# Kernel tuning notes

Measured on AMD Instinct MI355X. Metric: run time of the kernel, lower is better.

Reference implementation:

```python
import jax, jax.numpy as jnp
import numpy as np

N_TOTAL = 100000  # total nodes in feature table
N = 16384         # batch of center nodes
K = 32            # fixed neighbor count per relation
S = 16            # num_sample = ceil(K * threshold=0.5)
D = 190           # feat_dim (hard-coded in source weight)
E = 64            # embed_dim


def setup_inputs() -> dict:
    key = jax.random.key(0)
    ks = jax.random.split(key, 7)
    features = jax.random.normal(ks[0], (N_TOTAL, D), dtype=jnp.float32)
    nodes = jax.random.randint(ks[1], (N,), 0, N_TOTAL)
    neigh1 = jax.random.randint(ks[2], (N, K), 0, N_TOTAL)
    neigh2 = jax.random.randint(ks[3], (N, K), 0, N_TOTAL)
    neigh3 = jax.random.randint(ks[4], (N, K), 0, N_TOTAL)
    lim_w = float(np.sqrt(6.0 / (D + E)))  # xavier_uniform
    weight = jax.random.uniform(ks[5], (D, E), minval=-lim_w, maxval=lim_w, dtype=jnp.float32)
    lim_a = float(np.sqrt(6.0 / (2 * E + 1)))
    a = jax.random.uniform(ks[6], (2 * E, 1), minval=-lim_a, maxval=lim_a, dtype=jnp.float32)
    return {"features": features, "nodes": nodes, "neigh1": neigh1,
            "neigh2": neigh2, "neigh3": neigh3, "weight": weight, "a": a}


def _intra(features, nodes, neigh):
    """Cosine-similarity top-S neighbor filter + masked mean + relu (IntraAgg)."""
    center = features[nodes]                      # [N, D]
    nf = features[neigh]                          # [N, K, D] gather
    sim = jnp.einsum('nd,nkd->nk', center, nf)
    sim = sim / (jnp.linalg.norm(center, axis=1, keepdims=True)
                 * jnp.linalg.norm(nf, axis=2))   # cosine similarity [N, K]
    _, top_idx = jax.lax.top_k(sim, S)            # [N, S] most-similar neighbors
    sel = jnp.take_along_axis(nf, top_idx[:, :, None], axis=1)  # [N, S, D]
    return jax.nn.relu(sel.mean(axis=1))          # uniform average -> relu, [N, D]


def reference(features, nodes, neigh1, neigh2, neigh3, weight, a):
    r_feats = [_intra(features, nodes, nb) for nb in (neigh1, neigh2, neigh3)]
    self_feats = features[nodes]                  # [N, D]
    center_h = self_feats @ weight                # [N, E]
    neigh_h = jnp.stack([r @ weight for r in r_feats])  # [3, N, E]
    # cat(center_h, neigh_h) @ a == center_h @ a[:E] + neigh_h @ a[E:]
    a1, a2 = a[:E], a[E:]
    e = jax.nn.leaky_relu(center_h @ a1 + neigh_h @ a2, 0.2)  # [3, N, 1]
    att = jax.nn.softmax(e[..., 0].T, axis=1)     # [N, 3] (eval mode: no dropout)
    aggregated = jnp.einsum('nr,rne->ne', att, neigh_h)       # [N, E]
    return jax.nn.relu(center_h + aggregated)
```

## Files before the change

### kernel.cpp

```cpp
#include <hip/hip_runtime.h>

#define NTOTAL 100000
#define NNODES 16384
#define K 32
#define S 16
#define D 190
#define E 64
#define NREL 3

__device__ float g_invn[NTOTAL];
__device__ float g_wa[384];

__global__ __launch_bounds__(256) void norms_kernel(const float* __restrict__ features) {
    const int row  = blockIdx.x * 4 + (threadIdx.x >> 6);
    const int lane = threadIdx.x & 63;
    if (row >= NTOTAL) return;
    const float2* rp = (const float2*)(features + (size_t)row * D);
    float2 a = rp[lane];
    float ss = fmaf(a.x, a.x, a.y * a.y);
    if (lane < 31) {
        float2 b = rp[64 + lane];
        ss = fmaf(b.x, b.x, fmaf(b.y, b.y, ss));
    }
    #pragma unroll
    for (int off = 32; off; off >>= 1) ss += __shfl_xor(ss, off, 64);
    if (lane == 0) g_invn[row] = 1.0f / sqrtf(ss);
}

__global__ __launch_bounds__(192) void prep_wa(const float* __restrict__ weight,
                                               const float* __restrict__ avec) {
    const int d = threadIdx.x;
    float s1 = 0.f, s2 = 0.f;
    if (d < D) {
        const float* wr = weight + d * E;
        #pragma unroll 8
        for (int e = 0; e < E; ++e) {
            const float w = wr[e];
            s1 = fmaf(w, avec[e],     s1);
            s2 = fmaf(w, avec[E + e], s2);
        }
    }
    g_wa[d]       = s1;
    g_wa[192 + d] = s2;
}

__global__ __launch_bounds__(256) void interagg_wave(
    const float* __restrict__ features,
    const int*   __restrict__ nodes,
    const int*   __restrict__ neigh1,
    const int*   __restrict__ neigh2,
    const int*   __restrict__ neigh3,
    const float* __restrict__ weight,
    float*       __restrict__ out)
{
    __shared__ int   s_idx[4][96];
    __shared__ float s_sim[4][32];
    __shared__ __align__(16) float s_v[4][192];

    const int t    = threadIdx.x;
    const int lane = t & 63;
    const int wave = t >> 6;
    const int n    = blockIdx.x * 4 + wave;

    int*   idxw = s_idx[wave];
    float* simw = s_sim[wave];
    float* vw   = s_v[wave];

    {
        const int v1 = (lane < 32) ? neigh1[n * K + lane] : neigh2[n * K + (lane - 32)];
        idxw[lane] = v1;
        if (lane < 32) idxw[64 + lane] = neigh3[n * K + lane];
    }

    const int  crow = nodes[n];
    const int  hl   = (lane < 31) ? lane : 30;
    const bool hiok = (lane < 31);
    const float2* crp = (const float2*)(features + (size_t)crow * D);
    float2 c0 = crp[lane];
    float2 c1 = crp[64 + hl];
    if (!hiok) { c1.x = 0.f; c1.y = 0.f; }

    float rlx[NREL], rly[NREL], rhx[NREL], rhy[NREL];

    #pragma unroll
    for (int rel = 0; rel < NREL; ++rel) {
        const int* idz = idxw + rel * 32;

        #pragma unroll
        for (int b = 0; b < 4; ++b) {
            float2 va[8], vb[8];
            float  dt[8];
            #pragma unroll
            for (int i = 0; i < 8; ++i) {
                const int rid = idz[b * 8 + i];
                const float2* rp = (const float2*)(features + (size_t)rid * D);
                va[i] = rp[lane];
                vb[i] = rp[64 + hl];
            }
            #pragma unroll
            for (int i = 0; i < 8; ++i)
                dt[i] = fmaf(c0.x, va[i].x, fmaf(c0.y, va[i].y,
                        fmaf(c1.x, vb[i].x, c1.y * vb[i].y)));
            #pragma unroll
            for (int off = 32; off; off >>= 1) {
                #pragma unroll
                for (int i = 0; i < 8; ++i)
                    dt[i] += __shfl_xor(dt[i], off, 64);
            }
            if (lane == 0) {
                #pragma unroll
                for (int i = 0; i < 8; ++i)
                    simw[b * 8 + i] = dt[i];
            }
        }

        if (lane < 32) simw[lane] *= g_invn[idz[lane]];

        const float sk = simw[lane & 31];
        int rank = (lane < 32) ? 0 : 64;
        #pragma unroll
        for (int j = 0; j < K; ++j) {
            const float sj = __shfl(sk, j, 64);
            rank += (sj > sk) || (sj == sk && j < lane);
        }
        unsigned int m = (unsigned int)__ballot(rank < S);

        float2 acc_lo = make_float2(0.f, 0.f);
        float2 acc_hi = make_float2(0.f, 0.f);
        #pragma unroll
        for (int half = 0; half < 2; ++half) {
            float2 ua[8], ub[8];
            #pragma unroll
            for (int i = 0; i < 8; ++i) {
                const int k = __ffs(m) - 1; m &= m - 1;
                const int rid = idz[k];
                const float2* rp = (const float2*)(features + (size_t)rid * D);
                ua[i] = rp[lane];
                ub[i] = rp[64 + hl];
            }
            #pragma unroll
            for (int i = 0; i < 8; ++i) {
                acc_lo.x += ua[i].x; acc_lo.y += ua[i].y;
                acc_hi.x += ub[i].x; acc_hi.y += ub[i].y;
            }
        }
        rlx[rel] = fmaxf(acc_lo.x * (1.f / S), 0.f);
        rly[rel] = fmaxf(acc_lo.y * (1.f / S), 0.f);
        rhx[rel] = fmaxf(acc_hi.x * (1.f / S), 0.f);
        rhy[rel] = fmaxf(acc_hi.y * (1.f / S), 0.f);
    }

    float2 w1l = ((const float2*)g_wa)[lane];
    float2 w1h = ((const float2*)g_wa)[64 + hl];
    float2 w2l = ((const float2*)(g_wa + 192))[lane];
    float2 w2h = ((const float2*)(g_wa + 192))[64 + hl];
    if (!hiok) { w1h.x = w1h.y = 0.f; w2h.x = w2h.y = 0.f; }

    float dv[4];
    dv[0] = fmaf(c0.x, w1l.x, fmaf(c0.y, w1l.y, fmaf(c1.x, w1h.x, c1.y * w1h.y)));
    #pragma unroll
    for (int r = 0; r < NREL; ++r)
        dv[1 + r] = fmaf(rlx[r], w2l.x, fmaf(rly[r], w2l.y,
                    fmaf(rhx[r], w2h.x, rhy[r] * w2h.y)));
    #pragma unroll
    for (int off = 32; off; off >>= 1) {
        #pragma unroll
        for (int i = 0; i < 4; ++i)
            dv[i] += __shfl_xor(dv[i], off, 64);
    }

    float e1 = dv[0] + dv[1], e2 = dv[0] + dv[2], e3 = dv[0] + dv[3];
    e1 = (e1 >= 0.f) ? e1 : 0.2f * e1;
    e2 = (e2 >= 0.f) ? e2 : 0.2f * e2;
    e3 = (e3 >= 0.f) ? e3 : 0.2f * e3;
    const float mx  = fmaxf(e1, fmaxf(e2, e3));
    const float x1 = expf(e1 - mx), x2 = expf(e2 - mx), x3 = expf(e3 - mx);
    const float inv = 1.f / (x1 + x2 + x3);
    const float a1w = x1 * inv, a2w = x2 * inv, a3w = x3 * inv;

    float2 v_lo, v_hi;
    v_lo.x = fmaf(a1w, rlx[0], fmaf(a2w, rlx[1], fmaf(a3w, rlx[2], c0.x)));
    v_lo.y = fmaf(a1w, rly[0], fmaf(a2w, rly[1], fmaf(a3w, rly[2], c0.y)));
    v_hi.x = fmaf(a1w, rhx[0], fmaf(a2w, rhx[1], fmaf(a3w, rhx[2], c1.x)));
    v_hi.y = fmaf(a1w, rhy[0], fmaf(a2w, rhy[1], fmaf(a3w, rhy[2], c1.y)));

    ((float2*)vw)[lane] = v_lo;
    if (hiok) ((float2*)vw)[64 + lane] = v_hi;

    float acc = 0.f;
    const float* wcol = weight + lane;
    #pragma unroll 4
    for (int d4 = 0; d4 < 47; ++d4) {
        const float4 vv = *((const float4*)vw + d4);
        const int d = d4 * 4;
        acc = fmaf(vv.x, wcol[(d    ) * E], acc);
        acc = fmaf(vv.y, wcol[(d + 1) * E], acc);
        acc = fmaf(vv.z, wcol[(d + 2) * E], acc);
        acc = fmaf(vv.w, wcol[(d + 3) * E], acc);
    }
    {
        const float2 vv2 = *((const float2*)vw + 94);
        acc = fmaf(vv2.x, wcol[188 * E], acc);
        acc = fmaf(vv2.y, wcol[189 * E], acc);
    }
    out[(size_t)n * E + lane] = fmaxf(acc, 0.f);
}

extern "C" void kernel_launch(void* const* d_in, const int* in_sizes, int n_in,
                              void* d_out, int out_size, void* d_ws, size_t ws_size,
                              hipStream_t stream) {
    const float* features = (const float*)d_in[0];
    const int*   nodes    = (const int*)  d_in[1];
    const int*   neigh1   = (const int*)  d_in[2];
    const int*   neigh2   = (const int*)  d_in[3];
    const int*   neigh3   = (const int*)  d_in[4];
    const float* weight   = (const float*)d_in[5];
    const float* avec     = (const float*)d_in[6];
    float*       out      = (float*)d_out;

    norms_kernel<<<NTOTAL / 4, 256, 0, stream>>>(features);
    prep_wa<<<1, 192, 0, stream>>>(weight, avec);
    interagg_wave<<<NNODES / 4, 256, 0, stream>>>(
        features, nodes, neigh1, neigh2, neigh3, weight, out);
}
```

Before: 319.9 us.

## Pad feature rows to 192 floats in workspace and embed inverse norm

Adds a pre-pass that copies the feature table into a workspace with rows padded to 192 floats, storing each row's inverse norm in the padding slot. The main kernel gathers from the padded, aligned rows and takes the norm from a lane it already loads, so the separate norm lookup goes away. This costs an extra full-table write pass and depends on having enough workspace, with the old path kept as a fallback.

After: 468.3 us. 1.46x slower.

```diff
diff --git a/kernel.cpp b/kernel.cpp
--- a/kernel.cpp
+++ b/kernel.cpp
@@ -7,9 +7,29 @@
 #define D 190
 #define E 64
 #define NREL 3
+#define PROW 192
 
 __device__ float g_invn[NTOTAL];
 __device__ float g_wa[384];
+
+__global__ __launch_bounds__(256) void pad_kernel(const float* __restrict__ features,
+                                                  float* __restrict__ pf) {
+    const int row  = blockIdx.x * 4 + (threadIdx.x >> 6);
+    const int lane = threadIdx.x & 63;
+    if (row >= NTOTAL) return;
+    const float2* rp = (const float2*)(features + (size_t)row * D);
+    float2 lo = rp[lane];
+    float2 hi = make_float2(0.f, 0.f);
+    if (lane < 31) hi = rp[64 + lane];
+    float ss = fmaf(lo.x, lo.x, fmaf(lo.y, lo.y, fmaf(hi.x, hi.x, hi.y * hi.y)));
+    #pragma unroll
+    for (int off = 32; off; off >>= 1) ss += __shfl_xor(ss, off, 64);
+    const float invn = 1.0f / sqrtf(ss);
+    float2* wp = (float2*)(pf + (size_t)row * PROW);
+    wp[lane] = lo;
+    if (lane < 31) wp[64 + lane] = hi;
+    if (lane == 31) wp[95] = make_float2(invn, 0.f);
+}
 
 __global__ __launch_bounds__(256) void norms_kernel(const float* __restrict__ features) {
     const int row  = blockIdx.x * 4 + (threadIdx.x >> 6);
@@ -42,6 +62,167 @@
     }
     g_wa[d]       = s1;
     g_wa[192 + d] = s2;
+}
+
+__global__ __launch_bounds__(256) void interagg_pad(
+    const float* __restrict__ pf,
+    const int*   __restrict__ nodes,
+    const int*   __restrict__ neigh1,
+    const int*   __restrict__ neigh2,
+    const int*   __restrict__ neigh3,
+    const float* __restrict__ weight,
+    float*       __restrict__ out)
+{
+    __shared__ int   s_idx[4][96];
+    __shared__ float s_sim[4][32];
+    __shared__ __align__(16) float s_v[4][192];
+
+    const int t    = threadIdx.x;
+    const int lane = t & 63;
+    const int wave = t >> 6;
+    const int n    = blockIdx.x * 4 + wave;
+
+    int*   idxw = s_idx[wave];
+    float* simw = s_sim[wave];
+    float* vw   = s_v[wave];
+
+    {
+        const int v1 = (lane < 32) ? neigh1[n * K + lane] : neigh2[n * K + (lane - 32)];
+        idxw[lane] = v1;
+        if (lane < 32) idxw[64 + lane] = neigh3[n * K + lane];
+    }
+
+    const int  crow = nodes[n];
+    const bool hiok = (lane < 32);
+    const float2* crp = (const float2*)(pf + (size_t)crow * PROW);
+    float2 c0 = crp[lane];
+    float2 c1 = hiok ? crp[64 + lane] : make_float2(0.f, 0.f);
+    if (lane == 31) { c1.x = 0.f; c1.y = 0.f; }
+
+    float rlx[NREL], rly[NREL], rhx[NREL], rhy[NREL];
+
+    #pragma unroll
+    for (int rel = 0; rel < NREL; ++rel) {
+        const int* idz = idxw + rel * 32;
+
+        #pragma unroll
+        for (int b = 0; b < 4; ++b) {
+            float2 va[8], vb[8];
+            float  dt[8];
+            #pragma unroll
+            for (int i = 0; i < 8; ++i) {
+                const int rid = idz[b * 8 + i];
+                const float2* rp = (const float2*)(pf + (size_t)rid * PROW);
+                va[i] = rp[lane];
+                vb[i] = hiok ? rp[64 + lane] : make_float2(0.f, 0.f);
+            }
+            #pragma unroll
+            for (int i = 0; i < 8; ++i) {
+                dt[i] = fmaf(c0.x, va[i].x, fmaf(c0.y, va[i].y,
+                        fmaf(c1.x, vb[i].x, c1.y * vb[i].y)));
+            }
+            #pragma unroll
+            for (int off = 32; off; off >>= 1) {
+                #pragma unroll
+                for (int i = 0; i < 8; ++i)
+                    dt[i] += __shfl_xor(dt[i], off, 64);
+            }
+            if (lane == 31) {
+                #pragma unroll
+                for (int i = 0; i < 8; ++i)
+                    simw[b * 8 + i] = dt[i] * vb[i].x;
+            }
+        }
+
+        const float sk = simw[lane & 31];
+        int rank = (lane < 32) ? 0 : 64;
+        #pragma unroll
+        for (int j = 0; j < K; ++j) {
+            const float sj = __shfl(sk, j, 64);
+            rank += (sj > sk) || (sj == sk && j < lane);
+        }
+        unsigned int m = (unsigned int)__ballot(rank < S);
+
+        float2 acc_lo = make_float2(0.f, 0.f);
+        float2 acc_hi = make_float2(0.f, 0.f);
+        #pragma unroll
+        for (int half = 0; half < 2; ++half) {
+            float2 ua[8], ub[8];
+            #pragma unroll
+            for (int i = 0; i < 8; ++i) {
+                const int k = __ffs(m) - 1; m &= m - 1;
+                const int rid = idz[k];
+                const float2* rp = (const float2*)(pf + (size_t)rid * PROW);
+                ua[i] = rp[lane];
+                ub[i] = hiok ? rp[64 + lane] : make_float2(0.f, 0.f);
+            }
+            #pragma unroll
+            for (int i = 0; i < 8; ++i) {
+                acc_lo.x += ua[i].x; acc_lo.y += ua[i].y;
+                acc_hi.x += ub[i].x; acc_hi.y += ub[i].y;
+            }
+        }
+        rlx[rel] = fmaxf(acc_lo.x * (1.f / S), 0.f);
+        rly[rel] = fmaxf(acc_lo.y * (1.f / S), 0.f);
+        rhx[rel] = fmaxf(acc_hi.x * (1.f / S), 0.f);
+        rhy[rel] = fmaxf(acc_hi.y * (1.f / S), 0.f);
+    }
+
+    const float2* gw1 = (const float2*)g_wa;
+    const float2* gw2 = (const float2*)(g_wa + 192);
+    float2 w1l = gw1[lane];
+    float2 w1h = hiok ? gw1[64 + lane] : make_float2(0.f, 0.f);
+    float2 w2l = gw2[lane];
+    float2 w2h = hiok ? gw2[64 + lane] : make_float2(0.f, 0.f);
+
+    float dv[4];
+    dv[0] = fmaf(c0.x, w1l.x, fmaf(c0.y, w1l.y, fmaf(c1.x, w1h.x, c1.y * w1h.y)));
+    #pragma unroll
+    for (int r = 0; r < NREL; ++r)
+        dv[1 + r] = fmaf(rlx[r], w2l.x, fmaf(rly[r], w2l.y,
+                    fmaf(rhx[r], w2h.x, rhy[r] * w2h.y)));
+    #pragma unroll
+    for (int off = 32; off; off >>= 1) {
+        #pragma unroll
+        for (int i = 0; i < 4; ++i)
+            dv[i] += __shfl_xor(dv[i], off, 64);
+    }
+
+    float e1 = dv[0] + dv[1], e2 = dv[0] + dv[2], e3 = dv[0] + dv[3];
+    e1 = (e1 >= 0.f) ? e1 : 0.2f * e1;
+    e2 = (e2 >= 0.f) ? e2 : 0.2f * e2;
+    e3 = (e3 >= 0.f) ? e3 : 0.2f * e3;
+    const float mx  = fmaxf(e1, fmaxf(e2, e3));
+    const float x1 = expf(e1 - mx), x2 = expf(e2 - mx), x3 = expf(e3 - mx);
+    const float inv = 1.f / (x1 + x2 + x3);
+    const float a1w = x1 * inv, a2w = x2 * inv, a3w = x3 * inv;
+
+    float2 v_lo, v_hi;
+    v_lo.x = fmaf(a1w, rlx[0], fmaf(a2w, rlx[1], fmaf(a3w, rlx[2], c0.x)));
+    v_lo.y = fmaf(a1w, rly[0], fmaf(a2w, rly[1], fmaf(a3w, rly[2], c0.y)));
+    v_hi.x = fmaf(a1w, rhx[0], fmaf(a2w, rhx[1], fmaf(a3w, rhx[2], c1.x)));
+    v_hi.y = fmaf(a1w, rhy[0], fmaf(a2w, rhy[1], fmaf(a3w, rhy[2], c1.y)));
+
+    ((float2*)vw)[lane] = v_lo;
+    if (hiok) ((float2*)vw)[64 + lane] = v_hi;
+
+    float acc = 0.f;
+    const float* wcol = weight + lane;
+    #pragma unroll 4
+    for (int d4 = 0; d4 < 47; ++d4) {
+        const float4 vv = *((const float4*)vw + d4);
+        const int d = d4 * 4;
+        acc = fmaf(vv.x, wcol[(d    ) * E], acc);
+        acc = fmaf(vv.y, wcol[(d + 1) * E], acc);
+        acc = fmaf(vv.z, wcol[(d + 2) * E], acc);
+        acc = fmaf(vv.w, wcol[(d + 3) * E], acc);
+    }
+    {
+        const float2 vv2 = *((const float2*)vw + 94);
+        acc = fmaf(vv2.x, wcol[188 * E], acc);
+        acc = fmaf(vv2.y, wcol[189 * E], acc);
+    }
+    out[(size_t)n * E + lane] = fmaxf(acc, 0.f);
 }
 
 __global__ __launch_bounds__(256) void interagg_wave(
@@ -85,7 +266,6 @@
     #pragma unroll
     for (int rel = 0; rel < NREL; ++rel) {
         const int* idz = idxw + rel * 32;
-
         #pragma unroll
         for (int b = 0; b < 4; ++b) {
             float2 va[8], vb[8];
@@ -113,7 +293,6 @@
                     simw[b * 8 + i] = dt[i];
             }
         }
-
         if (lane < 32) simw[lane] *= g_invn[idz[lane]];
 
         const float sk = simw[lane & 31];
@@ -218,8 +397,17 @@
     const float* avec     = (const float*)d_in[6];
     float*       out      = (float*)d_out;
 
-    norms_kernel<<<NTOTAL / 4, 256, 0, stream>>>(features);
     prep_wa<<<1, 192, 0, stream>>>(weight, avec);
-    interagg_wave<<<NNODES / 4, 256, 0, stream>>>(
-        features, nodes, neigh1, neigh2, neigh3, weight, out);
-}
+
+    const bool padded = ws_size >= (size_t)NTOTAL * PROW * sizeof(float);
+    if (padded) {
+        float* pf = (float*)d_ws;
+        pad_kernel<<<NTOTAL / 4, 256, 0, stream>>>(features, pf);
+        interagg_pad<<<NNODES / 4, 256, 0, stream>>>(
+            pf, nodes, neigh1, neigh2, neigh3, weight, out);
+    } else {
+        norms_kernel<<<NTOTAL / 4, 256, 0, stream>>>(features);
+        interagg_wave<<<NNODES / 4, 256, 0, stream>>>(
+            features, nodes, neigh1, neigh2, neigh3, weight, out);
+    }
+}
```
